# Performance work log

Measured on AMD Instinct MI355X. Metric: run time of the kernel, lower is better.

## Reference

```python
import jax, jax.numpy as jnp
import numpy as np

N, DEG, F_IN, F_OUT = 50000, 16, 128, 128
E = N * DEG


def setup_inputs() -> dict:
    key = jax.random.key(0)
    k1, k2, k3 = jax.random.split(key, 3)
    x = jax.random.normal(k1, (N, F_IN), dtype=jnp.float32)
    # flat ragged neighbor features: edge e belongs to node seg_ids[e]
    neigh = jax.random.normal(k2, (E, F_IN), dtype=jnp.float32)
    seg_ids = (jnp.arange(E, dtype=jnp.int32) // DEG)  # sorted, each node has DEG neighbors
    # nn.Linear(in, out, bias=False) weight: [out_features, in_features]
    W = jax.random.normal(k3, (F_OUT, F_IN), dtype=jnp.float32) / np.sqrt(F_IN)
    return {"x": x, "neigh": neigh, "seg_ids": seg_ids, "W": W}


def reference(x, neigh, seg_ids, W):
    n = x.shape[0]
    # per-node mean of neighbor features (segment mean over ragged lists)
    ones = jnp.ones((neigh.shape[0],), dtype=x.dtype)
    counts = jax.ops.segment_sum(ones, seg_ids, num_segments=n)  # [N]
    f = jax.ops.segment_sum(neigh, seg_ids, num_segments=n) / counts[:, None]  # [N, F_in]
    # shared linear transform (no bias)
    x_out = (x + f) @ W.T          # [N, F_out]
    neigh_out = neigh @ W.T        # [E, F_out] (all ragged neighbor sets, flat)
    return (x_out, neigh_out)
```

## Files before the change

### kernel.cpp

```cpp
#include <hip/hip_runtime.h>
#include <hip/hip_bf16.h>

#define FDIM  128
#define GNODE 8
#define DEGC  16
#define TROWS 128
#define ROWB  256

typedef __attribute__((ext_vector_type(8))) short   bvec8;
typedef __attribute__((ext_vector_type(8))) __bf16  bf16v8;
typedef __attribute__((ext_vector_type(4))) float   fvec4;

__device__ __forceinline__ unsigned short f2bf(float f) {
    unsigned int u = __builtin_bit_cast(unsigned int, f);
    u += 0x7fffu + ((u >> 16) & 1u);
    return (unsigned short)(u >> 16);
}

__device__ __forceinline__ fvec4 mfma16(bvec8 a, bvec8 b, fvec4 c) {
    return __builtin_amdgcn_mfma_f32_16x16x32_bf16(
        __builtin_bit_cast(bf16v8, a), __builtin_bit_cast(bf16v8, b), c, 0, 0, 0);
}

__device__ __forceinline__ void st8(char* base, int row, int bir, bvec8 v) {
    *(bvec8*)(base + row * ROWB + (bir ^ ((row & 7) << 4))) = v;
}
__device__ __forceinline__ bvec8 ld8(const char* base, int row, int bir) {
    return *(const bvec8*)(base + row * ROWB + (bir ^ ((row & 7) << 4)));
}

__device__ __forceinline__ void stage_w(const float* __restrict__ W, char* lds_w, int t) {
    const int sl = t & 15, wr = t >> 4;
    #pragma unroll
    for (int i = 0; i < 8; ++i) {
        const int row = i * 16 + wr;
        const float4* p = (const float4*)(W + (size_t)row * FDIM + sl * 8);
        float4 lo = p[0], hi = p[1];
        float v[8] = {lo.x, lo.y, lo.z, lo.w, hi.x, hi.y, hi.z, hi.w};
        bvec8 o;
        #pragma unroll
        for (int c = 0; c < 8; ++c) o[c] = (short)f2bf(v[c]);
        st8(lds_w, row, sl * 16, o);
    }
}

__device__ __forceinline__ void tile_mm(const char* lds_in, const char* lds_w,
                                        int wave, int lane, fvec4 acc[2][8]) {
    const int lr = lane & 15, lg = lane >> 4;
    #pragma unroll
    for (int ks = 0; ks < 4; ++ks) {
        const int kb = ks * 64 + lg * 16;
        bvec8 a0 = ld8(lds_in, wave * 32 + lr,      kb);
        bvec8 a1 = ld8(lds_in, wave * 32 + 16 + lr, kb);
        #pragma unroll
        for (int tn = 0; tn < 8; ++tn) {
            bvec8 b = ld8(lds_w, tn * 16 + lr, kb);
            acc[0][tn] = mfma16(a0, b, acc[0][tn]);
            acc[1][tn] = mfma16(a1, b, acc[1][tn]);
        }
    }
}

__global__ __launch_bounds__(256, 2)
void gcn_main(const float* __restrict__ x, const float* __restrict__ neigh,
              const float* __restrict__ W,
              float* __restrict__ out_nb, bvec8* __restrict__ comb_ws)
{
    __shared__ __align__(16) char lds_in[TROWS * ROWB];
    __shared__ __align__(16) char lds_w [FDIM * ROWB];

    const int t    = threadIdx.x;
    const int blk  = blockIdx.x;
    const int g    = t >> 5;
    const int half = (t >> 4) & 1;
    const int sl   = t & 15;

    const float* nbase = neigh + ((size_t)(blk * GNODE + g) * DEGC) * FDIM + sl * 8;
    float acv[8];
    #pragma unroll
    for (int c = 0; c < 8; ++c) acv[c] = 0.f;

    #pragma unroll
    for (int s = 0; s < 8; ++s) {
        const int j = half * 8 + s;
        const float4* p = (const float4*)(nbase + (size_t)j * FDIM);
        float4 lo = p[0], hi = p[1];
        float v[8] = {lo.x, lo.y, lo.z, lo.w, hi.x, hi.y, hi.z, hi.w};
        bvec8 o;
        #pragma unroll
        for (int c = 0; c < 8; ++c) { acv[c] += v[c]; o[c] = (short)f2bf(v[c]); }
        st8(lds_in, g * DEGC + j, sl * 16, o);
    }
    #pragma unroll
    for (int c = 0; c < 8; ++c) acv[c] += __shfl_xor(acv[c], 16);

    if (half == 0) {
        const int node = blk * GNODE + g;
        const float4* p = (const float4*)(x + (size_t)node * FDIM + sl * 8);
        float4 lo = p[0], hi = p[1];
        float v[8] = {lo.x, lo.y, lo.z, lo.w, hi.x, hi.y, hi.z, hi.w};
        bvec8 o;
        #pragma unroll
        for (int c = 0; c < 8; ++c) o[c] = (short)f2bf(v[c] + acv[c] * (1.f / 16.f));
        comb_ws[(size_t)node * 16 + sl] = o;
    }

    stage_w(W, lds_w, t);
    __syncthreads();

    const int wave = t >> 6, lane = t & 63;
    const int lr = lane & 15, lg = lane >> 4;

    fvec4 acc[2][8];
    #pragma unroll
    for (int i = 0; i < 2; ++i)
        #pragma unroll
        for (int j = 0; j < 8; ++j) acc[i][j] = (fvec4){0.f, 0.f, 0.f, 0.f};

    tile_mm(lds_in, lds_w, wave, lane, acc);

    #pragma unroll
    for (int tm = 0; tm < 2; ++tm) {
        const size_t rbase = (size_t)blk * TROWS + wave * 32 + tm * 16 + lg * 4;
        #pragma unroll
        for (int tn = 0; tn < 8; ++tn)
            #pragma unroll
            for (int r = 0; r < 4; ++r)
                out_nb[(rbase + r) * FDIM + tn * 16 + lr] = acc[tm][tn][r];
    }
}

__global__ __launch_bounds__(256, 2)
void gcn_xout(const bvec8* __restrict__ comb_ws, const float* __restrict__ W,
              float* __restrict__ out_x, int n)
{
    __shared__ __align__(16) char lds_in[TROWS * ROWB];
    __shared__ __align__(16) char lds_w [FDIM * ROWB];

    const int t   = threadIdx.x;
    const int blk = blockIdx.x;
    const int sl  = t & 15;

    #pragma unroll
    for (int i = 0; i < 8; ++i) {
        const int row = i * 16 + (t >> 4);
        int src = blk * TROWS + row;
        if (src > n - 1) src = n - 1;
        bvec8 v = comb_ws[(size_t)src * 16 + sl];
        st8(lds_in, row, sl * 16, v);
    }

    stage_w(W, lds_w, t);
    __syncthreads();

    const int wave = t >> 6, lane = t & 63;
    const int lr = lane & 15, lg = lane >> 4;

    fvec4 acc[2][8];
    #pragma unroll
    for (int i = 0; i < 2; ++i)
        #pragma unroll
        for (int j = 0; j < 8; ++j) acc[i][j] = (fvec4){0.f, 0.f, 0.f, 0.f};

    tile_mm(lds_in, lds_w, wave, lane, acc);

    #pragma unroll
    for (int tm = 0; tm < 2; ++tm) {
        const int mbase = blk * TROWS + wave * 32 + tm * 16 + lg * 4;
        #pragma unroll
        for (int tn = 0; tn < 8; ++tn)
            #pragma unroll
            for (int r = 0; r < 4; ++r) {
                const int m = mbase + r;
                if (m < n)
                    out_x[(size_t)m * FDIM + tn * 16 + lr] = acc[tm][tn][r];
            }
    }
}

extern "C" void kernel_launch(void* const* d_in, const int* in_sizes, int n_in,
                              void* d_out, int out_size, void* d_ws, size_t ws_size,
                              hipStream_t stream) {
    const float* x     = (const float*)d_in[0];
    const float* neigh = (const float*)d_in[1];
    const float* W     = (const float*)d_in[3];

    const int n = in_sizes[0] / FDIM;
    float* out_x  = (float*)d_out;
    float* out_nb = out_x + (size_t)n * FDIM;
    bvec8* comb   = (bvec8*)d_ws;

    const int blocks1 = n / GNODE;
    hipLaunchKernelGGL(gcn_main, dim3(blocks1), dim3(256), 0, stream,
                       x, neigh, W, out_nb, comb);

    const int blocks2 = (n + TROWS - 1) / TROWS;
    hipLaunchKernelGGL(gcn_xout, dim3(blocks2), dim3(256), 0, stream,
                       comb, W, out_x, n);
}
```

Measured before the change: 184.7 us.

## Keep W fragments in registers per wave and drop W LDS staging

Each wave now owns two 16-column output tiles and loads its W fragments directly from global memory into registers, converting them to bf16 once. This replaces the shared W tile in LDS. It halves LDS use per block, which allows the launch bound to rise to three blocks per CU, and it removes W's LDS writes and B-fragment LDS reads. In exchange, every wave reads all 128 rows of the input tile from LDS, and the output stores are now split into 32-column strips per wave, which may coalesce less well.

```diff
diff --git a/kernel.cpp b/kernel.cpp
--- a/kernel.cpp
+++ b/kernel.cpp
@@ -29,45 +29,41 @@
     return *(const bvec8*)(base + row * ROWB + (bir ^ ((row & 7) << 4)));
 }
 
-__device__ __forceinline__ void stage_w(const float* __restrict__ W, char* lds_w, int t) {
-    const int sl = t & 15, wr = t >> 4;
-    #pragma unroll
-    for (int i = 0; i < 8; ++i) {
-        const int row = i * 16 + wr;
-        const float4* p = (const float4*)(W + (size_t)row * FDIM + sl * 8);
-        float4 lo = p[0], hi = p[1];
-        float v[8] = {lo.x, lo.y, lo.z, lo.w, hi.x, hi.y, hi.z, hi.w};
-        bvec8 o;
-        #pragma unroll
-        for (int c = 0; c < 8; ++c) o[c] = (short)f2bf(v[c]);
-        st8(lds_w, row, sl * 16, o);
-    }
-}
-
-__device__ __forceinline__ void tile_mm(const char* lds_in, const char* lds_w,
-                                        int wave, int lane, fvec4 acc[2][8]) {
-    const int lr = lane & 15, lg = lane >> 4;
-    #pragma unroll
-    for (int ks = 0; ks < 4; ++ks) {
-        const int kb = ks * 64 + lg * 16;
-        bvec8 a0 = ld8(lds_in, wave * 32 + lr,      kb);
-        bvec8 a1 = ld8(lds_in, wave * 32 + 16 + lr, kb);
-        #pragma unroll
-        for (int tn = 0; tn < 8; ++tn) {
-            bvec8 b = ld8(lds_w, tn * 16 + lr, kb);
-            acc[0][tn] = mfma16(a0, b, acc[0][tn]);
-            acc[1][tn] = mfma16(a1, b, acc[1][tn]);
+__device__ __forceinline__ bvec8 load_bfrag(const float* __restrict__ W,
+                                            int tn, int ks, int lr, int lg) {
+    const float4* p = (const float4*)(W + (size_t)(tn * 16 + lr) * FDIM + ks * 32 + lg * 8);
+    float4 lo = p[0], hi = p[1];
+    bvec8 o;
+    o[0] = (short)f2bf(lo.x); o[1] = (short)f2bf(lo.y);
+    o[2] = (short)f2bf(lo.z); o[3] = (short)f2bf(lo.w);
+    o[4] = (short)f2bf(hi.x); o[5] = (short)f2bf(hi.y);
+    o[6] = (short)f2bf(hi.z); o[7] = (short)f2bf(hi.w);
+    return o;
+}
+
+__device__ __forceinline__ void tile_mm2(const char* lds_in,
+                                         const bvec8 bA[4], const bvec8 bB[4],
+                                         int lr, int lg, fvec4 acc[8][2]) {
+    #pragma unroll
+    for (int mt = 0; mt < 8; ++mt) {
+        bvec8 a[4];
+        #pragma unroll
+        for (int ks = 0; ks < 4; ++ks)
+            a[ks] = ld8(lds_in, mt * 16 + lr, ks * 64 + lg * 16);
+        #pragma unroll
+        for (int ks = 0; ks < 4; ++ks) {
+            acc[mt][0] = mfma16(a[ks], bA[ks], acc[mt][0]);
+            acc[mt][1] = mfma16(a[ks], bB[ks], acc[mt][1]);
         }
     }
 }
 
-__global__ __launch_bounds__(256, 2)
+__global__ __launch_bounds__(256, 3)
 void gcn_main(const float* __restrict__ x, const float* __restrict__ neigh,
               const float* __restrict__ W,
               float* __restrict__ out_nb, bvec8* __restrict__ comb_ws)
 {
     __shared__ __align__(16) char lds_in[TROWS * ROWB];
-    __shared__ __align__(16) char lds_w [FDIM * ROWB];
 
     const int t    = threadIdx.x;
     const int blk  = blockIdx.x;
@@ -105,37 +101,42 @@
         comb_ws[(size_t)node * 16 + sl] = o;
     }
 
-    stage_w(W, lds_w, t);
-    __syncthreads();
-
     const int wave = t >> 6, lane = t & 63;
     const int lr = lane & 15, lg = lane >> 4;
-
-    fvec4 acc[2][8];
-    #pragma unroll
-    for (int i = 0; i < 2; ++i)
-        #pragma unroll
-        for (int j = 0; j < 8; ++j) acc[i][j] = (fvec4){0.f, 0.f, 0.f, 0.f};
-
-    tile_mm(lds_in, lds_w, wave, lane, acc);
-
-    #pragma unroll
-    for (int tm = 0; tm < 2; ++tm) {
-        const size_t rbase = (size_t)blk * TROWS + wave * 32 + tm * 16 + lg * 4;
-        #pragma unroll
-        for (int tn = 0; tn < 8; ++tn)
+    bvec8 bA[4], bB[4];
+    #pragma unroll
+    for (int ks = 0; ks < 4; ++ks) {
+        bA[ks] = load_bfrag(W, wave * 2,     ks, lr, lg);
+        bB[ks] = load_bfrag(W, wave * 2 + 1, ks, lr, lg);
+    }
+
+    __syncthreads();
+
+    fvec4 acc[8][2];
+    #pragma unroll
+    for (int i = 0; i < 8; ++i) {
+        acc[i][0] = (fvec4){0.f, 0.f, 0.f, 0.f};
+        acc[i][1] = (fvec4){0.f, 0.f, 0.f, 0.f};
+    }
+
+    tile_mm2(lds_in, bA, bB, lr, lg, acc);
+
+    #pragma unroll
+    for (int mt = 0; mt < 8; ++mt) {
+        const size_t rbase = (size_t)blk * TROWS + mt * 16 + lg * 4;
+        #pragma unroll
+        for (int j = 0; j < 2; ++j)
             #pragma unroll
             for (int r = 0; r < 4; ++r)
-                out_nb[(rbase + r) * FDIM + tn * 16 + lr] = acc[tm][tn][r];
-    }
-}
-
-__global__ __launch_bounds__(256, 2)
+                out_nb[(rbase + r) * FDIM + (wave * 2 + j) * 16 + lr] = acc[mt][j][r];
+    }
+}
+
+__global__ __launch_bounds__(256, 3)
 void gcn_xout(const bvec8* __restrict__ comb_ws, const float* __restrict__ W,
               float* __restrict__ out_x, int n)
 {
     __shared__ __align__(16) char lds_in[TROWS * ROWB];
-    __shared__ __align__(16) char lds_w [FDIM * ROWB];
 
     const int t   = threadIdx.x;
     const int blk = blockIdx.x;
@@ -150,30 +151,36 @@
         st8(lds_in, row, sl * 16, v);
     }
 
-    stage_w(W, lds_w, t);
-    __syncthreads();
-
     const int wave = t >> 6, lane = t & 63;
     const int lr = lane & 15, lg = lane >> 4;
-
-    fvec4 acc[2][8];
-    #pragma unroll
-    for (int i = 0; i < 2; ++i)
-        #pragma unroll
-        for (int j = 0; j < 8; ++j) acc[i][j] = (fvec4){0.f, 0.f, 0.f, 0.f};
-
-    tile_mm(lds_in, lds_w, wave, lane, acc);
-
-    #pragma unroll
-    for (int tm = 0; tm < 2; ++tm) {
-        const int mbase = blk * TROWS + wave * 32 + tm * 16 + lg * 4;
-        #pragma unroll
-        for (int tn = 0; tn < 8; ++tn)
+    bvec8 bA[4], bB[4];
+    #pragma unroll
+    for (int ks = 0; ks < 4; ++ks) {
+        bA[ks] = load_bfrag(W, wave * 2,     ks, lr, lg);
+        bB[ks] = load_bfrag(W, wave * 2 + 1, ks, lr, lg);
+    }
+
+    __syncthreads();
+
+    fvec4 acc[8][2];
+    #pragma unroll
+    for (int i = 0; i < 8; ++i) {
+        acc[i][0] = (fvec4){0.f, 0.f, 0.f, 0.f};
+        acc[i][1] = (fvec4){0.f, 0.f, 0.f, 0.f};
+    }
+
+    tile_mm2(lds_in, bA, bB, lr, lg, acc);
+
+    #pragma unroll
+    for (int mt = 0; mt < 8; ++mt) {
+        const int mbase = blk * TROWS + mt * 16 + lg * 4;
+        #pragma unroll
+        for (int j = 0; j < 2; ++j)
             #pragma unroll
             for (int r = 0; r < 4; ++r) {
                 const int m = mbase + r;
                 if (m < n)
-                    out_x[(size_t)m * FDIM + tn * 16 + lr] = acc[tm][tn][r];
+                    out_x[(size_t)m * FDIM + (wave * 2 + j) * 16 + lr] = acc[mt][j][r];
             }
     }
 }
```

Result: slower. 199.9 us (+8.2%).

## Compute neighbor mean from projected outputs and load A operands directly from global

Applied to the files above, without the earlier changes.

Uses linearity, mean(neigh)@W^T equals the mean of neigh@W^T, so the neighbor-mean projection is computed by reducing the MFMA accumulators across lanes. The result goes to the workspace as bf16 and is added in the x-output kernel, which now only multiplies x by W. The LDS staging of input rows is removed and A fragments are loaded and converted straight from global memory, which halves LDS use and raises the occupancy hint to 4. The costs are a bf16-rounded mean term added after the matmul and uncoalesced per-lane global loads.

```diff
diff --git a/kernel.cpp b/kernel.cpp
--- a/kernel.cpp
+++ b/kernel.cpp
@@ -11,12 +11,6 @@
 typedef __attribute__((ext_vector_type(8))) __bf16  bf16v8;
 typedef __attribute__((ext_vector_type(4))) float   fvec4;
 
-__device__ __forceinline__ unsigned short f2bf(float f) {
-    unsigned int u = __builtin_bit_cast(unsigned int, f);
-    u += 0x7fffu + ((u >> 16) & 1u);
-    return (unsigned short)(u >> 16);
-}
-
 __device__ __forceinline__ fvec4 mfma16(bvec8 a, bvec8 b, fvec4 c) {
     return __builtin_amdgcn_mfma_f32_16x16x32_bf16(
         __builtin_bit_cast(bf16v8, a), __builtin_bit_cast(bf16v8, b), c, 0, 0, 0);
@@ -29,29 +23,51 @@
     return *(const bvec8*)(base + row * ROWB + (bir ^ ((row & 7) << 4)));
 }
 
+__device__ __forceinline__ bvec8 ldcvt(const float* __restrict__ p) {
+    float4 lo = ((const float4*)p)[0], hi = ((const float4*)p)[1];
+    bf16v8 o;
+    o[0] = (__bf16)lo.x; o[1] = (__bf16)lo.y; o[2] = (__bf16)lo.z; o[3] = (__bf16)lo.w;
+    o[4] = (__bf16)hi.x; o[5] = (__bf16)hi.y; o[6] = (__bf16)hi.z; o[7] = (__bf16)hi.w;
+    return __builtin_bit_cast(bvec8, o);
+}
+
 __device__ __forceinline__ void stage_w(const float* __restrict__ W, char* lds_w, int t) {
     const int sl = t & 15, wr = t >> 4;
     #pragma unroll
     for (int i = 0; i < 8; ++i) {
         const int row = i * 16 + wr;
-        const float4* p = (const float4*)(W + (size_t)row * FDIM + sl * 8);
-        float4 lo = p[0], hi = p[1];
-        float v[8] = {lo.x, lo.y, lo.z, lo.w, hi.x, hi.y, hi.z, hi.w};
-        bvec8 o;
-        #pragma unroll
-        for (int c = 0; c < 8; ++c) o[c] = (short)f2bf(v[c]);
-        st8(lds_w, row, sl * 16, o);
+        st8(lds_w, row, sl * 16, ldcvt(W + (size_t)row * FDIM + sl * 8));
     }
 }
 
-__device__ __forceinline__ void tile_mm(const char* lds_in, const char* lds_w,
-                                        int wave, int lane, fvec4 acc[2][8]) {
+__global__ __launch_bounds__(256, 4)
+void gcn_main(const float* __restrict__ neigh, const float* __restrict__ W,
+              float* __restrict__ out_nb, __hip_bfloat16* __restrict__ nsum_ws)
+{
+    __shared__ __align__(16) char lds_w[FDIM * ROWB];
+
+    const int t    = threadIdx.x;
+    const int blk  = blockIdx.x;
+    const int wave = t >> 6, lane = t & 63;
     const int lr = lane & 15, lg = lane >> 4;
+
+    stage_w(W, lds_w, t);
+    __syncthreads();
+
+    const float* arow0 = neigh + ((size_t)blk * TROWS + wave * 32 + lr) * FDIM;
+    const float* arow1 = arow0 + 16 * FDIM;
+
+    fvec4 acc[2][8];
+    #pragma unroll
+    for (int i = 0; i < 2; ++i)
+        #pragma unroll
+        for (int j = 0; j < 8; ++j) acc[i][j] = (fvec4){0.f, 0.f, 0.f, 0.f};
+
     #pragma unroll
     for (int ks = 0; ks < 4; ++ks) {
+        bvec8 a0 = ldcvt(arow0 + ks * 32 + lg * 8);
+        bvec8 a1 = ldcvt(arow1 + ks * 32 + lg * 8);
         const int kb = ks * 64 + lg * 16;
-        bvec8 a0 = ld8(lds_in, wave * 32 + lr,      kb);
-        bvec8 a1 = ld8(lds_in, wave * 32 + 16 + lr, kb);
         #pragma unroll
         for (int tn = 0; tn < 8; ++tn) {
             bvec8 b = ld8(lds_w, tn * 16 + lr, kb);
@@ -59,65 +75,6 @@
             acc[1][tn] = mfma16(a1, b, acc[1][tn]);
         }
     }
-}
-
-__global__ __launch_bounds__(256, 2)
-void gcn_main(const float* __restrict__ x, const float* __restrict__ neigh,
-              const float* __restrict__ W,
-              float* __restrict__ out_nb, bvec8* __restrict__ comb_ws)
-{
-    __shared__ __align__(16) char lds_in[TROWS * ROWB];
-    __shared__ __align__(16) char lds_w [FDIM * ROWB];
-
-    const int t    = threadIdx.x;
-    const int blk  = blockIdx.x;
-    const int g    = t >> 5;
-    const int half = (t >> 4) & 1;
-    const int sl   = t & 15;
-
-    const float* nbase = neigh + ((size_t)(blk * GNODE + g) * DEGC) * FDIM + sl * 8;
-    float acv[8];
-    #pragma unroll
-    for (int c = 0; c < 8; ++c) acv[c] = 0.f;
-
-    #pragma unroll
-    for (int s = 0; s < 8; ++s) {
-        const int j = half * 8 + s;
-        const float4* p = (const float4*)(nbase + (size_t)j * FDIM);
-        float4 lo = p[0], hi = p[1];
-        float v[8] = {lo.x, lo.y, lo.z, lo.w, hi.x, hi.y, hi.z, hi.w};
-        bvec8 o;
-        #pragma unroll
-        for (int c = 0; c < 8; ++c) { acv[c] += v[c]; o[c] = (short)f2bf(v[c]); }
-        st8(lds_in, g * DEGC + j, sl * 16, o);
-    }
-    #pragma unroll
-    for (int c = 0; c < 8; ++c) acv[c] += __shfl_xor(acv[c], 16);
-
-    if (half == 0) {
-        const int node = blk * GNODE + g;
-        const float4* p = (const float4*)(x + (size_t)node * FDIM + sl * 8);
-        float4 lo = p[0], hi = p[1];
-        float v[8] = {lo.x, lo.y, lo.z, lo.w, hi.x, hi.y, hi.z, hi.w};
-        bvec8 o;
-        #pragma unroll
-        for (int c = 0; c < 8; ++c) o[c] = (short)f2bf(v[c] + acv[c] * (1.f / 16.f));
-        comb_ws[(size_t)node * 16 + sl] = o;
-    }
-
-    stage_w(W, lds_w, t);
-    __syncthreads();
-
-    const int wave = t >> 6, lane = t & 63;
-    const int lr = lane & 15, lg = lane >> 4;
-
-    fvec4 acc[2][8];
-    #pragma unroll
-    for (int i = 0; i < 2; ++i)
-        #pragma unroll
-        for (int j = 0; j < 8; ++j) acc[i][j] = (fvec4){0.f, 0.f, 0.f, 0.f};
-
-    tile_mm(lds_in, lds_w, wave, lane, acc);
 
     #pragma unroll
     for (int tm = 0; tm < 2; ++tm) {
@@ -128,33 +85,43 @@
             for (int r = 0; r < 4; ++r)
                 out_nb[(rbase + r) * FDIM + tn * 16 + lr] = acc[tm][tn][r];
     }
+
+    #pragma unroll
+    for (int tm = 0; tm < 2; ++tm) {
+        const int node = blk * GNODE + wave * 2 + tm;
+        #pragma unroll
+        for (int tn = 0; tn < 8; ++tn) {
+            float p = acc[tm][tn][0] + acc[tm][tn][1] + acc[tm][tn][2] + acc[tm][tn][3];
+            p += __shfl_xor(p, 16);
+            p += __shfl_xor(p, 32);
+            if (lg == 0)
+                nsum_ws[(size_t)node * FDIM + tn * 16 + lr] =
+                    __float2bfloat16(p * (1.f / 16.f));
+        }
+    }
 }
 
-__global__ __launch_bounds__(256, 2)
-void gcn_xout(const bvec8* __restrict__ comb_ws, const float* __restrict__ W,
+__global__ __launch_bounds__(256, 4)
+void gcn_xout(const float* __restrict__ x, const float* __restrict__ W,
+              const __hip_bfloat16* __restrict__ nsum_ws,
               float* __restrict__ out_x, int n)
 {
-    __shared__ __align__(16) char lds_in[TROWS * ROWB];
-    __shared__ __align__(16) char lds_w [FDIM * ROWB];
+    __shared__ __align__(16) char lds_w[FDIM * ROWB];
 
-    const int t   = threadIdx.x;
-    const int blk = blockIdx.x;
-    const int sl  = t & 15;
-
-    #pragma unroll
-    for (int i = 0; i < 8; ++i) {
-        const int row = i * 16 + (t >> 4);
-        int src = blk * TROWS + row;
-        if (src > n - 1) src = n - 1;
-        bvec8 v = comb_ws[(size_t)src * 16 + sl];
-        st8(lds_in, row, sl * 16, v);
-    }
+    const int t    = threadIdx.x;
+    const int blk  = blockIdx.x;
+    const int wave = t >> 6, lane = t & 63;
+    const int lr = lane & 15, lg = lane >> 4;
 
     stage_w(W, lds_w, t);
     __syncthreads();
 
-    const int wave = t >> 6, lane = t & 63;
-    const int lr = lane & 15, lg = lane >> 4;
+    int m0 = blk * TROWS + wave * 32 + lr;
+    int m1 = m0 + 16;
+    if (m0 > n - 1) m0 = n - 1;
+    if (m1 > n - 1) m1 = n - 1;
+    const float* arow0 = x + (size_t)m0 * FDIM;
+    const float* arow1 = x + (size_t)m1 * FDIM;
 
     fvec4 acc[2][8];
     #pragma unroll
@@ -162,18 +129,31 @@
         #pragma unroll
         for (int j = 0; j < 8; ++j) acc[i][j] = (fvec4){0.f, 0.f, 0.f, 0.f};
 
-    tile_mm(lds_in, lds_w, wave, lane, acc);
+    #pragma unroll
+    for (int ks = 0; ks < 4; ++ks) {
+        bvec8 a0 = ldcvt(arow0 + ks * 32 + lg * 8);
+        bvec8 a1 = ldcvt(arow1 + ks * 32 + lg * 8);
+        const int kb = ks * 64 + lg * 16;
+        #pragma unroll
+        for (int tn = 0; tn < 8; ++tn) {
+            bvec8 b = ld8(lds_w, tn * 16 + lr, kb);
+            acc[0][tn] = mfma16(a0, b, acc[0][tn]);
+            acc[1][tn] = mfma16(a1, b, acc[1][tn]);
+        }
+    }
 
     #pragma unroll
     for (int tm = 0; tm < 2; ++tm) {
-        const int mbase = blk * TROWS + wave * 32 + tm * 16 + lg * 4;
+        const size_t rbase = (size_t)blk * TROWS + wave * 32 + tm * 16 + lg * 4;
         #pragma unroll
         for (int tn = 0; tn < 8; ++tn)
             #pragma unroll
             for (int r = 0; r < 4; ++r) {
-                const int m = mbase + r;
-                if (m < n)
-                    out_x[(size_t)m * FDIM + tn * 16 + lr] = acc[tm][tn][r];
+                const size_t m = rbase + r;
+                if ((int)m < n) {
+                    const size_t idx = m * FDIM + tn * 16 + lr;
+                    out_x[idx] = acc[tm][tn][r] + __bfloat162float(nsum_ws[idx]);
+                }
             }
     }
 }
@@ -188,13 +168,13 @@
     const int n = in_sizes[0] / FDIM;
     float* out_x  = (float*)d_out;
     float* out_nb = out_x + (size_t)n * FDIM;
-    bvec8* comb   = (bvec8*)d_ws;
+    __hip_bfloat16* nsum = (__hip_bfloat16*)d_ws;
 
     const int blocks1 = n / GNODE;
     hipLaunchKernelGGL(gcn_main, dim3(blocks1), dim3(256), 0, stream,
-                       x, neigh, W, out_nb, comb);
+                       neigh, W, out_nb, nsum);
 
     const int blocks2 = (n + TROWS - 1) / TROWS;
     hipLaunchKernelGGL(gcn_xout, dim3(blocks2), dim3(256), 0, stream,
-                       comb, W, out_x, n);
+                       x, W, nsum, out_x, n);
 }
```

Result: slower. 206.1 us (+11.5%).
